# Performance work log

Measured on AMD Instinct MI355X. Metric: run time of the kernel, lower is better.

The kernel has to match this reference:

```python
import jax, jax.numpy as jnp
import numpy as np

H = W = 56; WS = 7; SHIFT = 3; HEADS = 4; DIM = 128
HD = DIM // HEADS; SCALE = HD ** -0.5
NW = (H // WS) * (W // WS)  # 64 windows per image
N = WS * WS                 # 49 tokens per window
HID = int(DIM * 4.0)


def _rel_index():
    coords = np.stack(np.meshgrid(np.arange(WS), np.arange(WS), indexing='ij'))  # (2,WS,WS)
    cf = coords.reshape(2, -1)
    rel = (cf[:, :, None] - cf[:, None, :]).transpose(1, 2, 0)  # (N,N,2)
    rel[:, :, 0] += WS - 1
    rel[:, :, 1] += WS - 1
    rel[:, :, 0] *= 2 * WS - 1
    return jnp.asarray(rel.sum(-1))  # (N,N) int indices into bias table


def _attn_mask():
    img = np.zeros((H, W))
    cnt = 0
    for hs in (slice(0, -WS), slice(-WS, -SHIFT), slice(-SHIFT, None)):
        for ws in (slice(0, -WS), slice(-WS, -SHIFT), slice(-SHIFT, None)):
            img[hs, ws] = cnt
            cnt += 1
    mw = img.reshape(H // WS, WS, W // WS, WS).transpose(0, 2, 1, 3).reshape(-1, N)
    diff = mw[:, None, :] - mw[:, :, None]
    return jnp.asarray(np.where(diff != 0, -100.0, 0.0).astype(np.float32))  # (NW,N,N)

REL_IDX = _rel_index()
ATTN_MASK = _attn_mask()


def _ln(x, g, b):
    m = jnp.mean(x, -1, keepdims=True)
    v = jnp.var(x, -1, keepdims=True)
    return (x - m) * jax.lax.rsqrt(v + 1e-5) * g + b


def _win_part(x):  # (B,H,W,C) -> (B*NW, N, C)
    B = x.shape[0]
    x = x.reshape(B, H // WS, WS, W // WS, WS, DIM)
    return x.transpose(0, 1, 3, 2, 4, 5).reshape(-1, N, DIM)


def _win_rev(x, B):  # (B*NW, N, C) -> (B,H,W,C)
    x = x.reshape(B, H // WS, W // WS, WS, WS, DIM)
    return x.transpose(0, 1, 3, 2, 4, 5).reshape(B, H, W, DIM)


def setup_inputs() -> dict:
    key = jax.random.key(0)
    ks = jax.random.split(key, 8)
    s = 0.02
    return {
        'x': jax.random.normal(ks[0], (64, H * W, DIM), jnp.float32),
        'g1': jnp.ones((DIM,), jnp.float32),
        'b1': jnp.zeros((DIM,), jnp.float32),
        'qkv_w': jax.random.normal(ks[1], (3 * DIM, DIM), jnp.float32) * s,
        'qkv_b': jnp.zeros((3 * DIM,), jnp.float32),
        'rpb_table': jax.random.normal(ks[2], ((2 * WS - 1) ** 2, HEADS), jnp.float32) * s,
        'proj_w': jax.random.normal(ks[3], (DIM, DIM), jnp.float32) * s,
        'proj_b': jnp.zeros((DIM,), jnp.float32),
        'g2': jnp.ones((DIM,), jnp.float32),
        'b2': jnp.zeros((DIM,), jnp.float32),
        'fc1_w': jax.random.normal(ks[4], (HID, DIM), jnp.float32) * s,
        'fc1_b': jnp.zeros((HID,), jnp.float32),
        'fc2_w': jax.random.normal(ks[5], (DIM, HID), jnp.float32) * s,
        'fc2_b': jnp.zeros((DIM,), jnp.float32),
    }


def reference(x, g1, b1, qkv_w, qkv_b, rpb_table, proj_w, proj_b, g2, b2, fc1_w, fc1_b, fc2_w, fc2_b):
    B = x.shape[0]
    shortcut = x
    h = _ln(x, g1, b1).reshape(B, H, W, DIM)
    # cyclic shift + window partition
    h = jnp.roll(h, shift=(-SHIFT, -SHIFT), axis=(1, 2))
    xw = _win_part(h)  # (B*NW, N, C)
    B_ = xw.shape[0]
    # window attention
    qkv = (xw @ qkv_w.T + qkv_b).reshape(B_, N, 3, HEADS, HD).transpose(2, 0, 3, 1, 4)
    q, k, v = qkv[0] * SCALE, qkv[1], qkv[2]  # (B_, heads, N, hd)
    attn = jnp.einsum('bhnd,bhmd->bhnm', q, k)
    bias = rpb_table[REL_IDX.reshape(-1)].reshape(N, N, HEADS).transpose(2, 0, 1)  # (heads,N,N)
    attn = attn + bias[None]
    attn = attn.reshape(B, NW, HEADS, N, N) + ATTN_MASK[None, :, None]
    attn = jax.nn.softmax(attn.reshape(B_, HEADS, N, N), axis=-1)
    out = jnp.einsum('bhnm,bhmd->bhnd', attn, v).transpose(0, 2, 1, 3).reshape(B_, N, DIM)
    out = out @ proj_w.T + proj_b
    # reverse windows + reverse shift
    h = _win_rev(out, B)
    h = jnp.roll(h, shift=(SHIFT, SHIFT), axis=(1, 2)).reshape(B, H * W, DIM)
    x = shortcut + h
    # MLP
    y = _ln(x, g2, b2)
    y = jax.nn.gelu(y @ fc1_w.T + fc1_b, approximate=False)
    y = y @ fc2_w.T + fc2_b
    return x + y
```

## Files before the change

### kernel.cpp

```cpp
#include <hip/hip_runtime.h>

typedef unsigned int uint;
typedef unsigned short ushort;
using short8 = __attribute__((ext_vector_type(8))) short;
using f32x4  = __attribute__((ext_vector_type(4))) float;
using uint4v = __attribute__((ext_vector_type(4))) uint;

#define SCALE_ 0.17677669529663687f
#define MFMA(a,b,c) __builtin_amdgcn_mfma_f32_16x16x32_bf16(a,b,c,0,0,0)

__device__ inline ushort f2bf(float f){
  uint u = __float_as_uint(f);
  return (ushort)((u + 0x7fffu + ((u >> 16) & 1u)) >> 16);
}
__device__ inline uint pk2(float a, float b){
  return (uint)f2bf(a) | ((uint)f2bf(b) << 16);
}
__device__ inline float gelu(float v){
  return 0.5f * v * (1.f + erff(v * 0.70710678f));
}

__global__ __launch_bounds__(256) void prep_kernel(
    const float* __restrict__ qkv_w, const float* __restrict__ qkv_b,
    const float* __restrict__ rpb, const float* __restrict__ proj_w,
    const float* __restrict__ fc1_w, const float* __restrict__ fc2_w,
    ushort* __restrict__ qkv_wb, float* __restrict__ qkv_bs,
    ushort* __restrict__ proj_wb, ushort* __restrict__ fc1_wb,
    ushort* __restrict__ fc2_wb, ushort* __restrict__ T2b)
{
  int i = blockIdx.x * 256 + threadIdx.x;
  if (i < 49152) qkv_wb[i] = f2bf(qkv_w[i] * (i < 16384 ? SCALE_ : 1.f));
  if (i < 16384) proj_wb[i] = f2bf(proj_w[i]);
  if (i < 65536) { fc1_wb[i] = f2bf(fc1_w[i]); fc2_wb[i] = f2bf(fc2_w[i]); }
  if (i < 384)   qkv_bs[i] = qkv_b[i] * (i < 128 ? SCALE_ : 1.f);
  if (i < 65536) {
    int cls = i >> 14, h = (i >> 12) & 3, tok = (i >> 6) & 63, key = i & 63;
    float val = -30000.f;
    if (tok < 49 && key < 49) {
      int ri = tok / 7, ci = tok - ri * 7, rj = key / 7, cj = key - rj * 7;
      val = rpb[((ri - rj + 6) * 13 + (ci - cj + 6)) * 4 + h];
      int er = cls >> 1, ec = cls & 1;
      int regi = (er ? (ri < 4 ? 1 : 2) : 0) * 3 + (ec ? (ci < 4 ? 1 : 2) : 0);
      int regj = (er ? (rj < 4 ? 1 : 2) : 0) * 3 + (ec ? (cj < 4 ? 1 : 2) : 0);
      if (regi != regj) val -= 100.f;
    }
    T2b[i] = f2bf(val);
  }
}

__global__ __launch_bounds__(256, 2) void attn_kernel(
    const float* __restrict__ x, const float* __restrict__ g1, const float* __restrict__ b1,
    const ushort* __restrict__ qkv_wb, const float* __restrict__ qkv_bs,
    const ushort* __restrict__ T2b, const ushort* __restrict__ proj_wb,
    const float* __restrict__ proj_b, float* __restrict__ x_new)
{
  __shared__ __align__(16) char smem[25088];
  char*   xls = smem;
  ushort* oa  = (ushort*)smem;
  float*  Rp  = (float*)smem;
  const int tid = threadIdx.x;
  const int w = tid >> 6, lane = tid & 63;
  const int g = lane >> 4, li = lane & 15;
  const int blk = blockIdx.x;
  const int b = blk >> 6, wi = blk & 63;
  const int wr = wi >> 3, wc = wi & 7;
  const float* xb = x + (size_t)b * (3136 * 128);
  const f32x4 zf = {0.f, 0.f, 0.f, 0.f};
  const int srcA = ((g & 1) << 5) + li;
  const int srcB = srcA + 16;
  const int hi = g >> 1;

#pragma unroll
  for (int it = 0; it < 7; ++it) {
    int gi = it * 256 + tid;
    bool ok = gi < 1568;
    int t = ok ? (gi >> 5) : 48;
    int ch4 = (gi & 31) << 2;
    int tr = t / 7, tc = t - tr * 7;
    int rr = wr * 7 + tr + 3; rr -= (rr >= 56) ? 56 : 0;
    int cc = wc * 7 + tc + 3; cc -= (cc >= 56) ? 56 : 0;
    float4 v = *(const float4*)(xb + (size_t)(rr * 56 + cc) * 128 + ch4);
    float s = v.x + v.y + v.z + v.w;
    float s2 = v.x*v.x + v.y*v.y + v.z*v.z + v.w*v.w;
#pragma unroll
    for (int off = 16; off; off >>= 1) { s += __shfl_xor(s, off); s2 += __shfl_xor(s2, off); }
    float mn = s * 0.0078125f;
    float rs = rsqrtf(s2 * 0.0078125f - mn * mn + 1e-5f);
    if (ok) {
      float4 gg = *(const float4*)(g1 + ch4);
      float4 bb = *(const float4*)(b1 + ch4);
      uint2 u;
      u.x = pk2((v.x - mn) * rs * gg.x + bb.x, (v.y - mn) * rs * gg.y + bb.y);
      u.y = pk2((v.z - mn) * rs * gg.z + bb.z, (v.w - mn) * rs * gg.w + bb.w);
      int slot = ch4 >> 3;
      int tokx = t ^ ((slot & 7) << 1);
      *(uint2*)(xls + (slot * 64 + tokx) * 16 + ((ch4 & 4) << 1)) = u;
    }
  }
  if (tid < 240) {
    int slot = tid & 15, t = 49 + (tid >> 4);
    int tokx = t ^ ((slot & 7) << 1);
    uint4 z = make_uint4(0u, 0u, 0u, 0u);
    *(uint4*)(xls + (slot * 64 + tokx) * 16) = z;
  }
  __syncthreads();

  short8 kf[4];
  {
    f32x4 kacc[2][4];
#pragma unroll
    for (int cf = 0; cf < 2; ++cf)
#pragma unroll
      for (int m = 0; m < 4; ++m) kacc[cf][m] = zf;
#pragma unroll
    for (int kt = 0; kt < 4; ++kt) {
      const int slot = kt * 4 + g;
      short8 xf[4];
#pragma unroll
      for (int m = 0; m < 4; ++m)
        xf[m] = *(const short8*)(xls + (slot * 64 + ((m * 16 + li) ^ ((slot & 7) << 1))) * 16);
      const int wofs = kt * 32 + g * 8;
#pragma unroll
      for (int cf = 0; cf < 2; ++cf) {
        short8 wk = *(const short8*)(qkv_wb + (size_t)(128 + w * 32 + cf * 16 + li) * 128 + wofs);
#pragma unroll
        for (int m = 0; m < 4; ++m) kacc[cf][m] = MFMA(wk, xf[m], kacc[cf][m]);
      }
    }
    uint2 kp[2][4];
#pragma unroll
    for (int cf = 0; cf < 2; ++cf) {
      f32x4 kb4 = *(const f32x4*)(qkv_bs + 128 + w * 32 + cf * 16 + g * 4);
#pragma unroll
      for (int m = 0; m < 4; ++m) {
        f32x4 kv = kacc[cf][m] + kb4;
        kp[cf][m].x = pk2(kv[0], kv[1]); kp[cf][m].y = pk2(kv[2], kv[3]);
      }
    }
#pragma unroll
    for (int n = 0; n < 4; ++n) {
      uint a0 = __shfl(kp[0][n].x, srcA), a1 = __shfl(kp[0][n].y, srcA);
      uint a2 = __shfl(kp[0][n].x, srcB), a3 = __shfl(kp[0][n].y, srcB);
      uint b0 = __shfl(kp[1][n].x, srcA), b1 = __shfl(kp[1][n].y, srcA);
      uint b2 = __shfl(kp[1][n].x, srcB), b3 = __shfl(kp[1][n].y, srcB);
      uint4v u = { hi ? b0 : a0, hi ? b1 : a1, hi ? b2 : a2, hi ? b3 : a3 };
      kf[n] = __builtin_bit_cast(short8, u);
    }
  }

  short8 vt[2][2];
  {
    f32x4 vacc[4][2];
#pragma unroll
    for (int m = 0; m < 4; ++m) { vacc[m][0] = zf; vacc[m][1] = zf; }
#pragma unroll
    for (int kt = 0; kt < 4; ++kt) {
      const int slot = kt * 4 + g;
      short8 xf[4];
#pragma unroll
      for (int m = 0; m < 4; ++m)
        xf[m] = *(const short8*)(xls + (slot * 64 + ((m * 16 + li) ^ ((slot & 7) << 1))) * 16);
      const int wofs = kt * 32 + g * 8;
#pragma unroll
      for (int cf = 0; cf < 2; ++cf) {
        short8 wv = *(const short8*)(qkv_wb + (size_t)(256 + w * 32 + cf * 16 + li) * 128 + wofs);
#pragma unroll
        for (int m = 0; m < 4; ++m) vacc[m][cf] = MFMA(xf[m], wv, vacc[m][cf]);
      }
    }
    uint2 vp[4][2];
#pragma unroll
    for (int cf = 0; cf < 2; ++cf) {
      float vb = qkv_bs[256 + w * 32 + cf * 16 + li];
#pragma unroll
      for (int m = 0; m < 4; ++m) {
        f32x4 vv = vacc[m][cf];
        vp[m][cf].x = pk2(vv[0] + vb, vv[1] + vb);
        vp[m][cf].y = pk2(vv[2] + vb, vv[3] + vb);
      }
    }
#pragma unroll
    for (int kt = 0; kt < 2; ++kt)
#pragma unroll
      for (int half = 0; half < 2; ++half) {
        uint a0 = __shfl(vp[kt * 2][half].x, srcA), a1 = __shfl(vp[kt * 2][half].y, srcA);
        uint a2 = __shfl(vp[kt * 2][half].x, srcB), a3 = __shfl(vp[kt * 2][half].y, srcB);
        uint b0 = __shfl(vp[kt * 2 + 1][half].x, srcA), b1 = __shfl(vp[kt * 2 + 1][half].y, srcA);
        uint b2 = __shfl(vp[kt * 2 + 1][half].x, srcB), b3 = __shfl(vp[kt * 2 + 1][half].y, srcB);
        uint4v uv = { hi ? b0 : a0, hi ? b1 : a1, hi ? b2 : a2, hi ? b3 : a3 };
        vt[kt][half] = __builtin_bit_cast(short8, uv);
      }
  }

  f32x4 oacc[2][4];
#pragma unroll
  for (int cf = 0; cf < 2; ++cf)
#pragma unroll
    for (int m = 0; m < 4; ++m) oacc[cf][m] = zf;
  {
    const int cls = ((wr == 7) ? 2 : 0) | ((wc == 7) ? 1 : 0);
    const ushort* Tb = T2b + ((cls * 4 + w) << 12);
    const f32x4 qb40 = *(const f32x4*)(qkv_bs + w * 32 + g * 4);
    const f32x4 qb41 = *(const f32x4*)(qkv_bs + w * 32 + 16 + g * 4);
#pragma unroll
    for (int m = 0; m < 4; ++m) {
      f32x4 qacc[2] = {zf, zf};
#pragma unroll
      for (int kt = 0; kt < 4; ++kt) {
        const int slot = kt * 4 + g;
        short8 xfm = *(const short8*)(xls + (slot * 64 + ((m * 16 + li) ^ ((slot & 7) << 1))) * 16);
        const int wofs = kt * 32 + g * 8;
        short8 wq0 = *(const short8*)(qkv_wb + (size_t)(w * 32 + li) * 128 + wofs);
        short8 wq1 = *(const short8*)(qkv_wb + (size_t)(w * 32 + 16 + li) * 128 + wofs);
        qacc[0] = MFMA(wq0, xfm, qacc[0]);
        qacc[1] = MFMA(wq1, xfm, qacc[1]);
      }
      uint2 qpm[2];
      {
        f32x4 q0 = qacc[0] + qb40;
        f32x4 q1 = qacc[1] + qb41;
        qpm[0].x = pk2(q0[0], q0[1]); qpm[0].y = pk2(q0[2], q0[3]);
        qpm[1].x = pk2(q1[0], q1[1]); qpm[1].y = pk2(q1[2], q1[3]);
      }
      uint a0 = __shfl(qpm[0].x, srcA), a1 = __shfl(qpm[0].y, srcA);
      uint a2 = __shfl(qpm[0].x, srcB), a3 = __shfl(qpm[0].y, srcB);
      uint b0 = __shfl(qpm[1].x, srcA), b1 = __shfl(qpm[1].y, srcA);
      uint b2 = __shfl(qpm[1].x, srcB), b3 = __shfl(qpm[1].y, srcB);
      uint4v uq = { hi ? b0 : a0, hi ? b1 : a1, hi ? b2 : a2, hi ? b3 : a3 };
      short8 qf = __builtin_bit_cast(short8, uq);
      f32x4 s[4];
#pragma unroll
      for (int n = 0; n < 4; ++n) {
        s[n] = MFMA(kf[n], qf, zf);
        uint2 tv = *(const uint2*)(Tb + (m * 16 + li) * 64 + n * 16 + g * 4);
        s[n][0] += __uint_as_float(tv.x << 16);
        s[n][1] += __uint_as_float(tv.x & 0xffff0000u);
        s[n][2] += __uint_as_float(tv.y << 16);
        s[n][3] += __uint_as_float(tv.y & 0xffff0000u);
      }
      float mx = -3.4e38f;
#pragma unroll
      for (int n = 0; n < 4; ++n)
        mx = fmaxf(mx, fmaxf(fmaxf(s[n][0], s[n][1]), fmaxf(s[n][2], s[n][3])));
      mx = fmaxf(mx, __shfl_xor(mx, 16));
      mx = fmaxf(mx, __shfl_xor(mx, 32));
      float sum = 0.f;
#pragma unroll
      for (int n = 0; n < 4; ++n)
#pragma unroll
        for (int r = 0; r < 4; ++r) { float e = __expf(s[n][r] - mx); s[n][r] = e; sum += e; }
      sum += __shfl_xor(sum, 16); sum += __shfl_xor(sum, 32);
      float rsm = 1.f / sum;
      uint um[4][2];
#pragma unroll
      for (int n = 0; n < 4; ++n) {
        um[n][0] = pk2(s[n][0] * rsm, s[n][1] * rsm);
        um[n][1] = pk2(s[n][2] * rsm, s[n][3] * rsm);
      }
#pragma unroll
      for (int kt = 0; kt < 2; ++kt) {
        uint t00 = __shfl(um[kt * 2][0], srcA),  t10 = __shfl(um[kt * 2 + 1][0], srcA);
        uint t01 = __shfl(um[kt * 2][1], srcA),  t11 = __shfl(um[kt * 2 + 1][1], srcA);
        uint t02 = __shfl(um[kt * 2][0], srcB),  t12 = __shfl(um[kt * 2 + 1][0], srcB);
        uint t03 = __shfl(um[kt * 2][1], srcB),  t13 = __shfl(um[kt * 2 + 1][1], srcB);
        uint4v pu = { hi ? t10 : t00, hi ? t11 : t01, hi ? t12 : t02, hi ? t13 : t03 };
        short8 pf = __builtin_bit_cast(short8, pu);
        oacc[0][m] = MFMA(vt[kt][0], pf, oacc[0][m]);
        oacc[1][m] = MFMA(vt[kt][1], pf, oacc[1][m]);
      }
    }
  }
  __syncthreads();
#pragma unroll
  for (int cf = 0; cf < 2; ++cf)
#pragma unroll
    for (int m = 0; m < 4; ++m) {
      uint2 ou; ou.x = pk2(oacc[cf][m][0], oacc[cf][m][1]);
      ou.y = pk2(oacc[cf][m][2], oacc[cf][m][3]);
      *(uint2*)((char*)oa + ((m * 16 + li) * 136 + w * 32 + cf * 16 + g * 4) * 2) = ou;
    }
  __syncthreads();

  f32x4 pacc[2][4];
#pragma unroll
  for (int cf = 0; cf < 2; ++cf)
#pragma unroll
    for (int m = 0; m < 4; ++m) pacc[cf][m] = zf;
#pragma unroll
  for (int kt = 0; kt < 4; ++kt) {
    short8 af[4];
#pragma unroll
    for (int m = 0; m < 4; ++m)
      af[m] = *(const short8*)((char*)oa + (m * 16 + li) * 272 + kt * 64 + g * 16);
#pragma unroll
    for (int cf = 0; cf < 2; ++cf) {
      short8 wp = *(const short8*)(proj_wb + (size_t)(w * 32 + cf * 16 + li) * 128 + kt * 32 + g * 8);
#pragma unroll
      for (int m = 0; m < 4; ++m) pacc[cf][m] = MFMA(af[m], wp, pacc[cf][m]);
    }
  }
  __syncthreads();
#pragma unroll
  for (int cf = 0; cf < 2; ++cf) {
    int col = w * 32 + cf * 16 + li;
    float pb = proj_b[col];
#pragma unroll
    for (int m = 0; m < 4; ++m)
#pragma unroll
      for (int r = 0; r < 4; ++r) {
        int t2 = m * 16 + g * 4 + r;
        if (t2 < 49)
          Rp[t2 * 128 + (col ^ ((t2 & 7) << 2))] = pacc[cf][m][r] + pb;
      }
  }
  __syncthreads();

#pragma unroll
  for (int it = 0; it < 7; ++it) {
    int gi = it * 256 + tid;
    if (gi < 1568) {
      int t = gi >> 5, ch4 = (gi & 31) << 2;
      int tr = t / 7, tc = t - tr * 7;
      int rr = wr * 7 + tr + 3; rr -= (rr >= 56) ? 56 : 0;
      int cc = wc * 7 + tc + 3; cc -= (cc >= 56) ? 56 : 0;
      size_t off = ((size_t)b * 3136 + rr * 56 + cc) * 128 + ch4;
      f32x4 d = *(const f32x4*)&Rp[t * 128 + (ch4 ^ ((t & 7) << 2))];
      float4 xr = *(const float4*)(x + off);
      float4 ov;
      ov.x = xr.x + d[0]; ov.y = xr.y + d[1];
      ov.z = xr.z + d[2]; ov.w = xr.w + d[3];
      *(float4*)(x_new + off) = ov;
    }
  }
}

__global__ __launch_bounds__(256, 2) void mlp_kernel(
    float* __restrict__ xio,
    const float* __restrict__ g2, const float* __restrict__ b2,
    const ushort* __restrict__ w1, const float* __restrict__ fb1,
    const ushort* __restrict__ w2, const float* __restrict__ fb2)
{
  __shared__ __align__(16) char smem[32768];
  char* Axs = smem;
  char* hls = smem + 16384;
  float* Rp = (float*)smem;
  const int tid = threadIdx.x, lane = tid & 63, w = tid >> 6;
  const int g = lane >> 4, li = lane & 15;
  float* xw = xio + (size_t)blockIdx.x * 64 * 128;
  const f32x4 zf = {0.f, 0.f, 0.f, 0.f};

#pragma unroll
  for (int it = 0; it < 8; ++it) {
    int gi = it * 256 + tid;
    int row = gi >> 5, ch4 = (gi & 31) << 2;
    float4 v = *(const float4*)(xw + row * 128 + ch4);
    float s = v.x + v.y + v.z + v.w;
    float s2 = v.x*v.x + v.y*v.y + v.z*v.z + v.w*v.w;
#pragma unroll
    for (int off = 16; off; off >>= 1) { s += __shfl_xor(s, off); s2 += __shfl_xor(s2, off); }
    float mn = s * 0.0078125f;
    float rs = rsqrtf(s2 * 0.0078125f - mn * mn + 1e-5f);
    float4 gg = *(const float4*)(g2 + ch4);
    float4 bb = *(const float4*)(b2 + ch4);
    uint2 u;
    u.x = pk2((v.x - mn) * rs * gg.x + bb.x, (v.y - mn) * rs * gg.y + bb.y);
    u.y = pk2((v.z - mn) * rs * gg.z + bb.z, (v.w - mn) * rs * gg.w + bb.w);
    int slot = ch4 >> 3;
    int tokx = row ^ ((slot & 7) << 1);
    *(uint2*)(Axs + (slot * 64 + tokx) * 16 + ((ch4 & 4) << 1)) = u;
  }
  __syncthreads();

  f32x4 acc2[4][2];
#pragma unroll
  for (int mi = 0; mi < 4; ++mi) { acc2[mi][0] = zf; acc2[mi][1] = zf; }

  for (int ck = 0; ck < 4; ++ck) {
    f32x4 acc1[2][4];
#pragma unroll
    for (int oi = 0; oi < 2; ++oi)
#pragma unroll
      for (int mi = 0; mi < 4; ++mi) acc1[oi][mi] = zf;
#pragma unroll
    for (int kt = 0; kt < 4; ++kt) {
      const int slot = kt * 4 + g;
      short8 xf[4];
#pragma unroll
      for (int mi = 0; mi < 4; ++mi)
        xf[mi] = *(const short8*)(Axs + (slot * 64 + ((mi * 16 + li) ^ ((slot & 7) << 1))) * 16);
#pragma unroll
      for (int oi = 0; oi < 2; ++oi) {
        short8 wf = *(const short8*)(w1 + (size_t)(ck * 128 + w * 32 + oi * 16 + li) * 128 + kt * 32 + g * 8);
#pragma unroll
        for (int mi = 0; mi < 4; ++mi) acc1[oi][mi] = MFMA(wf, xf[mi], acc1[oi][mi]);
      }
    }
#pragma unroll
    for (int oi = 0; oi < 2; ++oi) {
      f32x4 b4 = *(const f32x4*)(fb1 + ck * 128 + w * 32 + oi * 16 + g * 4);
#pragma unroll
      for (int mi = 0; mi < 4; ++mi) {
        f32x4 h = acc1[oi][mi] + b4;
        uint2 u; u.x = pk2(gelu(h[0]), gelu(h[1])); u.y = pk2(gelu(h[2]), gelu(h[3]));
        *(uint2*)(hls + ((w * 4 + oi * 2 + (g >> 1)) * 64 + mi * 16 + li) * 16 + ((g & 1) << 3)) = u;
      }
    }
    __syncthreads();
#pragma unroll
    for (int kt = 0; kt < 4; ++kt) {
      short8 hf[4];
#pragma unroll
      for (int mi = 0; mi < 4; ++mi)
        hf[mi] = *(const short8*)(hls + ((kt * 4 + g) * 64 + mi * 16 + li) * 16);
#pragma unroll
      for (int bo = 0; bo < 2; ++bo) {
        short8 wf = *(const short8*)(w2 + (size_t)(w * 32 + bo * 16 + li) * 512 + ck * 128 + kt * 32 + g * 8);
#pragma unroll
        for (int mi = 0; mi < 4; ++mi) acc2[mi][bo] = MFMA(hf[mi], wf, acc2[mi][bo]);
      }
    }
    __syncthreads();
  }

#pragma unroll
  for (int mi = 0; mi < 4; ++mi)
#pragma unroll
    for (int bo = 0; bo < 2; ++bo) {
      int out = w * 32 + bo * 16 + li;
#pragma unroll
      for (int r = 0; r < 4; ++r) {
        int tok = mi * 16 + g * 4 + r;
        Rp[tok * 128 + (out ^ ((tok & 7) << 2))] = acc2[mi][bo][r];
      }
    }
  __syncthreads();
#pragma unroll
  for (int it = 0; it < 8; ++it) {
    int gi = it * 256 + tid;
    int row = gi >> 5, ch4 = (gi & 31) << 2;
    f32x4 d = *(const f32x4*)&Rp[row * 128 + (ch4 ^ ((row & 7) << 2))];
    float4 xr = *(const float4*)(xw + row * 128 + ch4);
    float4 bb = *(const float4*)(fb2 + ch4);
    float4 ov;
    ov.x = xr.x + d[0] + bb.x; ov.y = xr.y + d[1] + bb.y;
    ov.z = xr.z + d[2] + bb.z; ov.w = xr.w + d[3] + bb.w;
    *(float4*)(xw + row * 128 + ch4) = ov;
  }
}

extern "C" void kernel_launch(void* const* d_in, const int* in_sizes, int n_in,
                              void* d_out, int out_size, void* d_ws, size_t ws_size,
                              hipStream_t stream)
{
  const float* x      = (const float*)d_in[0];
  const float* g1     = (const float*)d_in[1];
  const float* b1     = (const float*)d_in[2];
  const float* qkv_w  = (const float*)d_in[3];
  const float* qkv_b  = (const float*)d_in[4];
  const float* rpb    = (const float*)d_in[5];
  const float* proj_w = (const float*)d_in[6];
  const float* proj_b = (const float*)d_in[7];
  const float* g2     = (const float*)d_in[8];
  const float* b2     = (const float*)d_in[9];
  const float* fc1_w  = (const float*)d_in[10];
  const float* fc1_b  = (const float*)d_in[11];
  const float* fc2_w  = (const float*)d_in[12];
  const float* fc2_b  = (const float*)d_in[13];

  char* ws = (char*)d_ws;
  ushort* T2b     = (ushort*)ws;
  ushort* qkv_wb  = (ushort*)(ws + 262144);
  ushort* proj_wb = (ushort*)(ws + 360448);
  ushort* fc1_wb  = (ushort*)(ws + 393216);
  ushort* fc2_wb  = (ushort*)(ws + 524288);
  float*  qkv_bs  = (float*)(ws + 655360);
  float* out = (float*)d_out;

  prep_kernel<<<256, 256, 0, stream>>>(qkv_w, qkv_b, rpb, proj_w, fc1_w, fc2_w,
                                       qkv_wb, qkv_bs, proj_wb, fc1_wb, fc2_wb, T2b);
  attn_kernel<<<4096, 256, 0, stream>>>(x, g1, b1, qkv_wb, qkv_bs, T2b,
                                        proj_wb, proj_b, out);
  mlp_kernel<<<3136, 256, 0, stream>>>(out, g2, b2, fc1_wb, fc1_b, fc2_wb, fc2_b);
}
```

Before: 317.1 us.

## Run window attention with one wavefront per window, looping over heads

The attention kernel now launches 64 threads per block, and one wavefront processes all four heads of a window in sequence. Block-wide barriers go away, and the head outputs are regrouped with cross-lane shuffles for the projection instead of being staged through shared memory. The projection result is now kept in shared memory as bf16 rather than fp32, which shrinks shared memory use but adds rounding before the residual add. The cost is more serial work per wave, higher register pressure from holding all heads' outputs, and possibly lower occupancy or latency hiding.

```diff
diff --git a/kernel.cpp b/kernel.cpp
--- a/kernel.cpp
+++ b/kernel.cpp
@@ -16,6 +16,8 @@
 __device__ inline uint pk2(float a, float b){
   return (uint)f2bf(a) | ((uint)f2bf(b) << 16);
 }
+__device__ inline float bf2f_lo(uint u){ return __uint_as_float(u << 16); }
+__device__ inline float bf2f_hi(uint u){ return __uint_as_float(u & 0xffff0000u); }
 __device__ inline float gelu(float v){
   return 0.5f * v * (1.f + erff(v * 0.70710678f));
 }
@@ -48,18 +50,16 @@
   }
 }
 
-__global__ __launch_bounds__(256, 2) void attn_kernel(
+__global__ __launch_bounds__(64, 2) void attn_kernel(
     const float* __restrict__ x, const float* __restrict__ g1, const float* __restrict__ b1,
     const ushort* __restrict__ qkv_wb, const float* __restrict__ qkv_bs,
     const ushort* __restrict__ T2b, const ushort* __restrict__ proj_wb,
     const float* __restrict__ proj_b, float* __restrict__ x_new)
 {
-  __shared__ __align__(16) char smem[25088];
+  __shared__ __align__(16) char smem[16384];
   char*   xls = smem;
-  ushort* oa  = (ushort*)smem;
-  float*  Rp  = (float*)smem;
-  const int tid = threadIdx.x;
-  const int w = tid >> 6, lane = tid & 63;
+  ushort* Rpb = (ushort*)smem;
+  const int lane = threadIdx.x;
   const int g = lane >> 4, li = lane & 15;
   const int blk = blockIdx.x;
   const int b = blk >> 6, wi = blk & 63;
@@ -69,10 +69,11 @@
   const int srcA = ((g & 1) << 5) + li;
   const int srcB = srcA + 16;
   const int hi = g >> 1;
-
-#pragma unroll
-  for (int it = 0; it < 7; ++it) {
-    int gi = it * 256 + tid;
+  const int cls = ((wr == 7) ? 2 : 0) | ((wc == 7) ? 1 : 0);
+
+#pragma unroll
+  for (int it = 0; it < 25; ++it) {
+    int gi = it * 64 + lane;
     bool ok = gi < 1568;
     int t = ok ? (gi >> 5) : 48;
     int ch4 = (gi & 31) << 2;
@@ -97,238 +98,251 @@
       *(uint2*)(xls + (slot * 64 + tokx) * 16 + ((ch4 & 4) << 1)) = u;
     }
   }
-  if (tid < 240) {
-    int slot = tid & 15, t = 49 + (tid >> 4);
-    int tokx = t ^ ((slot & 7) << 1);
-    uint4 z = make_uint4(0u, 0u, 0u, 0u);
-    *(uint4*)(xls + (slot * 64 + tokx) * 16) = z;
-  }
-  __syncthreads();
-
-  short8 kf[4];
-  {
-    f32x4 kacc[2][4];
-#pragma unroll
-    for (int cf = 0; cf < 2; ++cf)
-#pragma unroll
-      for (int m = 0; m < 4; ++m) kacc[cf][m] = zf;
-#pragma unroll
-    for (int kt = 0; kt < 4; ++kt) {
-      const int slot = kt * 4 + g;
-      short8 xf[4];
-#pragma unroll
-      for (int m = 0; m < 4; ++m)
-        xf[m] = *(const short8*)(xls + (slot * 64 + ((m * 16 + li) ^ ((slot & 7) << 1))) * 16);
-      const int wofs = kt * 32 + g * 8;
-#pragma unroll
-      for (int cf = 0; cf < 2; ++cf) {
-        short8 wk = *(const short8*)(qkv_wb + (size_t)(128 + w * 32 + cf * 16 + li) * 128 + wofs);
-#pragma unroll
-        for (int m = 0; m < 4; ++m) kacc[cf][m] = MFMA(wk, xf[m], kacc[cf][m]);
-      }
-    }
-    uint2 kp[2][4];
-#pragma unroll
-    for (int cf = 0; cf < 2; ++cf) {
-      f32x4 kb4 = *(const f32x4*)(qkv_bs + 128 + w * 32 + cf * 16 + g * 4);
-#pragma unroll
-      for (int m = 0; m < 4; ++m) {
-        f32x4 kv = kacc[cf][m] + kb4;
-        kp[cf][m].x = pk2(kv[0], kv[1]); kp[cf][m].y = pk2(kv[2], kv[3]);
-      }
-    }
-#pragma unroll
-    for (int n = 0; n < 4; ++n) {
-      uint a0 = __shfl(kp[0][n].x, srcA), a1 = __shfl(kp[0][n].y, srcA);
-      uint a2 = __shfl(kp[0][n].x, srcB), a3 = __shfl(kp[0][n].y, srcB);
-      uint b0 = __shfl(kp[1][n].x, srcA), b1 = __shfl(kp[1][n].y, srcA);
-      uint b2 = __shfl(kp[1][n].x, srcB), b3 = __shfl(kp[1][n].y, srcB);
-      uint4v u = { hi ? b0 : a0, hi ? b1 : a1, hi ? b2 : a2, hi ? b3 : a3 };
-      kf[n] = __builtin_bit_cast(short8, u);
-    }
-  }
-
-  short8 vt[2][2];
-  {
-    f32x4 vacc[4][2];
-#pragma unroll
-    for (int m = 0; m < 4; ++m) { vacc[m][0] = zf; vacc[m][1] = zf; }
-#pragma unroll
-    for (int kt = 0; kt < 4; ++kt) {
-      const int slot = kt * 4 + g;
-      short8 xf[4];
-#pragma unroll
-      for (int m = 0; m < 4; ++m)
-        xf[m] = *(const short8*)(xls + (slot * 64 + ((m * 16 + li) ^ ((slot & 7) << 1))) * 16);
-      const int wofs = kt * 32 + g * 8;
-#pragma unroll
-      for (int cf = 0; cf < 2; ++cf) {
-        short8 wv = *(const short8*)(qkv_wb + (size_t)(256 + w * 32 + cf * 16 + li) * 128 + wofs);
-#pragma unroll
-        for (int m = 0; m < 4; ++m) vacc[m][cf] = MFMA(xf[m], wv, vacc[m][cf]);
-      }
-    }
-    uint2 vp[4][2];
-#pragma unroll
-    for (int cf = 0; cf < 2; ++cf) {
-      float vb = qkv_bs[256 + w * 32 + cf * 16 + li];
-#pragma unroll
-      for (int m = 0; m < 4; ++m) {
-        f32x4 vv = vacc[m][cf];
-        vp[m][cf].x = pk2(vv[0] + vb, vv[1] + vb);
-        vp[m][cf].y = pk2(vv[2] + vb, vv[3] + vb);
-      }
-    }
-#pragma unroll
-    for (int kt = 0; kt < 2; ++kt)
-#pragma unroll
-      for (int half = 0; half < 2; ++half) {
-        uint a0 = __shfl(vp[kt * 2][half].x, srcA), a1 = __shfl(vp[kt * 2][half].y, srcA);
-        uint a2 = __shfl(vp[kt * 2][half].x, srcB), a3 = __shfl(vp[kt * 2][half].y, srcB);
-        uint b0 = __shfl(vp[kt * 2 + 1][half].x, srcA), b1 = __shfl(vp[kt * 2 + 1][half].y, srcA);
-        uint b2 = __shfl(vp[kt * 2 + 1][half].x, srcB), b3 = __shfl(vp[kt * 2 + 1][half].y, srcB);
-        uint4v uv = { hi ? b0 : a0, hi ? b1 : a1, hi ? b2 : a2, hi ? b3 : a3 };
-        vt[kt][half] = __builtin_bit_cast(short8, uv);
-      }
-  }
-
-  f32x4 oacc[2][4];
-#pragma unroll
-  for (int cf = 0; cf < 2; ++cf)
-#pragma unroll
-    for (int m = 0; m < 4; ++m) oacc[cf][m] = zf;
-  {
-    const int cls = ((wr == 7) ? 2 : 0) | ((wc == 7) ? 1 : 0);
-    const ushort* Tb = T2b + ((cls * 4 + w) << 12);
-    const f32x4 qb40 = *(const f32x4*)(qkv_bs + w * 32 + g * 4);
-    const f32x4 qb41 = *(const f32x4*)(qkv_bs + w * 32 + 16 + g * 4);
-#pragma unroll
-    for (int m = 0; m < 4; ++m) {
-      f32x4 qacc[2] = {zf, zf};
+#pragma unroll
+  for (int i0 = 0; i0 < 4; ++i0) {
+    int i = i0 * 64 + lane;
+    if (i < 240) {
+      int slot = i & 15, t = 49 + (i >> 4);
+      int tokx = t ^ ((slot & 7) << 1);
+      uint4 z = make_uint4(0u, 0u, 0u, 0u);
+      *(uint4*)(xls + (slot * 64 + tokx) * 16) = z;
+    }
+  }
+
+  uint2 opk[4][4][2];
+#pragma unroll
+  for (int h = 0; h < 4; ++h) {
+    short8 kf[4];
+    {
+      f32x4 kacc[2][4];
+#pragma unroll
+      for (int cf = 0; cf < 2; ++cf)
+#pragma unroll
+        for (int m = 0; m < 4; ++m) kacc[cf][m] = zf;
 #pragma unroll
       for (int kt = 0; kt < 4; ++kt) {
         const int slot = kt * 4 + g;
-        short8 xfm = *(const short8*)(xls + (slot * 64 + ((m * 16 + li) ^ ((slot & 7) << 1))) * 16);
+        short8 xf[4];
+#pragma unroll
+        for (int m = 0; m < 4; ++m)
+          xf[m] = *(const short8*)(xls + (slot * 64 + ((m * 16 + li) ^ ((slot & 7) << 1))) * 16);
         const int wofs = kt * 32 + g * 8;
-        short8 wq0 = *(const short8*)(qkv_wb + (size_t)(w * 32 + li) * 128 + wofs);
-        short8 wq1 = *(const short8*)(qkv_wb + (size_t)(w * 32 + 16 + li) * 128 + wofs);
-        qacc[0] = MFMA(wq0, xfm, qacc[0]);
-        qacc[1] = MFMA(wq1, xfm, qacc[1]);
-      }
-      uint2 qpm[2];
-      {
-        f32x4 q0 = qacc[0] + qb40;
-        f32x4 q1 = qacc[1] + qb41;
-        qpm[0].x = pk2(q0[0], q0[1]); qpm[0].y = pk2(q0[2], q0[3]);
-        qpm[1].x = pk2(q1[0], q1[1]); qpm[1].y = pk2(q1[2], q1[3]);
-      }
-      uint a0 = __shfl(qpm[0].x, srcA), a1 = __shfl(qpm[0].y, srcA);
-      uint a2 = __shfl(qpm[0].x, srcB), a3 = __shfl(qpm[0].y, srcB);
-      uint b0 = __shfl(qpm[1].x, srcA), b1 = __shfl(qpm[1].y, srcA);
-      uint b2 = __shfl(qpm[1].x, srcB), b3 = __shfl(qpm[1].y, srcB);
-      uint4v uq = { hi ? b0 : a0, hi ? b1 : a1, hi ? b2 : a2, hi ? b3 : a3 };
-      short8 qf = __builtin_bit_cast(short8, uq);
-      f32x4 s[4];
+#pragma unroll
+        for (int cf = 0; cf < 2; ++cf) {
+          short8 wk = *(const short8*)(qkv_wb + (size_t)(128 + h * 32 + cf * 16 + li) * 128 + wofs);
+#pragma unroll
+          for (int m = 0; m < 4; ++m) kacc[cf][m] = MFMA(wk, xf[m], kacc[cf][m]);
+        }
+      }
+      uint2 kp[2][4];
+#pragma unroll
+      for (int cf = 0; cf < 2; ++cf) {
+        f32x4 kb4 = *(const f32x4*)(qkv_bs + 128 + h * 32 + cf * 16 + g * 4);
+#pragma unroll
+        for (int m = 0; m < 4; ++m) {
+          f32x4 kv = kacc[cf][m] + kb4;
+          kp[cf][m].x = pk2(kv[0], kv[1]); kp[cf][m].y = pk2(kv[2], kv[3]);
+        }
+      }
 #pragma unroll
       for (int n = 0; n < 4; ++n) {
-        s[n] = MFMA(kf[n], qf, zf);
-        uint2 tv = *(const uint2*)(Tb + (m * 16 + li) * 64 + n * 16 + g * 4);
-        s[n][0] += __uint_as_float(tv.x << 16);
-        s[n][1] += __uint_as_float(tv.x & 0xffff0000u);
-        s[n][2] += __uint_as_float(tv.y << 16);
-        s[n][3] += __uint_as_float(tv.y & 0xffff0000u);
-      }
-      float mx = -3.4e38f;
-#pragma unroll
-      for (int n = 0; n < 4; ++n)
-        mx = fmaxf(mx, fmaxf(fmaxf(s[n][0], s[n][1]), fmaxf(s[n][2], s[n][3])));
-      mx = fmaxf(mx, __shfl_xor(mx, 16));
-      mx = fmaxf(mx, __shfl_xor(mx, 32));
-      float sum = 0.f;
-#pragma unroll
-      for (int n = 0; n < 4; ++n)
-#pragma unroll
-        for (int r = 0; r < 4; ++r) { float e = __expf(s[n][r] - mx); s[n][r] = e; sum += e; }
-      sum += __shfl_xor(sum, 16); sum += __shfl_xor(sum, 32);
-      float rsm = 1.f / sum;
-      uint um[4][2];
-#pragma unroll
-      for (int n = 0; n < 4; ++n) {
-        um[n][0] = pk2(s[n][0] * rsm, s[n][1] * rsm);
-        um[n][1] = pk2(s[n][2] * rsm, s[n][3] * rsm);
-      }
-#pragma unroll
-      for (int kt = 0; kt < 2; ++kt) {
-        uint t00 = __shfl(um[kt * 2][0], srcA),  t10 = __shfl(um[kt * 2 + 1][0], srcA);
-        uint t01 = __shfl(um[kt * 2][1], srcA),  t11 = __shfl(um[kt * 2 + 1][1], srcA);
-        uint t02 = __shfl(um[kt * 2][0], srcB),  t12 = __shfl(um[kt * 2 + 1][0], srcB);
-        uint t03 = __shfl(um[kt * 2][1], srcB),  t13 = __shfl(um[kt * 2 + 1][1], srcB);
-        uint4v pu = { hi ? t10 : t00, hi ? t11 : t01, hi ? t12 : t02, hi ? t13 : t03 };
-        short8 pf = __builtin_bit_cast(short8, pu);
-        oacc[0][m] = MFMA(vt[kt][0], pf, oacc[0][m]);
-        oacc[1][m] = MFMA(vt[kt][1], pf, oacc[1][m]);
-      }
-    }
-  }
-  __syncthreads();
-#pragma unroll
-  for (int cf = 0; cf < 2; ++cf)
-#pragma unroll
-    for (int m = 0; m < 4; ++m) {
-      uint2 ou; ou.x = pk2(oacc[cf][m][0], oacc[cf][m][1]);
-      ou.y = pk2(oacc[cf][m][2], oacc[cf][m][3]);
-      *(uint2*)((char*)oa + ((m * 16 + li) * 136 + w * 32 + cf * 16 + g * 4) * 2) = ou;
-    }
-  __syncthreads();
-
-  f32x4 pacc[2][4];
-#pragma unroll
-  for (int cf = 0; cf < 2; ++cf)
-#pragma unroll
-    for (int m = 0; m < 4; ++m) pacc[cf][m] = zf;
-#pragma unroll
-  for (int kt = 0; kt < 4; ++kt) {
-    short8 af[4];
+        uint a0 = __shfl(kp[0][n].x, srcA), a1 = __shfl(kp[0][n].y, srcA);
+        uint a2 = __shfl(kp[0][n].x, srcB), a3 = __shfl(kp[0][n].y, srcB);
+        uint b0 = __shfl(kp[1][n].x, srcA), b1 = __shfl(kp[1][n].y, srcA);
+        uint b2 = __shfl(kp[1][n].x, srcB), b3 = __shfl(kp[1][n].y, srcB);
+        uint4v u = { hi ? b0 : a0, hi ? b1 : a1, hi ? b2 : a2, hi ? b3 : a3 };
+        kf[n] = __builtin_bit_cast(short8, u);
+      }
+    }
+    short8 vt[2][2];
+    {
+      f32x4 vacc[4][2];
+#pragma unroll
+      for (int m = 0; m < 4; ++m) { vacc[m][0] = zf; vacc[m][1] = zf; }
+#pragma unroll
+      for (int kt = 0; kt < 4; ++kt) {
+        const int slot = kt * 4 + g;
+        short8 xf[4];
+#pragma unroll
+        for (int m = 0; m < 4; ++m)
+          xf[m] = *(const short8*)(xls + (slot * 64 + ((m * 16 + li) ^ ((slot & 7) << 1))) * 16);
+        const int wofs = kt * 32 + g * 8;
+#pragma unroll
+        for (int cf = 0; cf < 2; ++cf) {
+          short8 wv = *(const short8*)(qkv_wb + (size_t)(256 + h * 32 + cf * 16 + li) * 128 + wofs);
+#pragma unroll
+          for (int m = 0; m < 4; ++m) vacc[m][cf] = MFMA(xf[m], wv, vacc[m][cf]);
+        }
+      }
+      uint2 vp[4][2];
+#pragma unroll
+      for (int cf = 0; cf < 2; ++cf) {
+        float vb = qkv_bs[256 + h * 32 + cf * 16 + li];
+#pragma unroll
+        for (int m = 0; m < 4; ++m) {
+          f32x4 vv = vacc[m][cf];
+          vp[m][cf].x = pk2(vv[0] + vb, vv[1] + vb);
+          vp[m][cf].y = pk2(vv[2] + vb, vv[3] + vb);
+        }
+      }
+#pragma unroll
+      for (int kt = 0; kt < 2; ++kt)
+#pragma unroll
+        for (int half = 0; half < 2; ++half) {
+          uint a0 = __shfl(vp[kt * 2][half].x, srcA), a1 = __shfl(vp[kt * 2][half].y, srcA);
+          uint a2 = __shfl(vp[kt * 2][half].x, srcB), a3 = __shfl(vp[kt * 2][half].y, srcB);
+          uint b0 = __shfl(vp[kt * 2 + 1][half].x, srcA), b1 = __shfl(vp[kt * 2 + 1][half].y, srcA);
+          uint b2 = __shfl(vp[kt * 2 + 1][half].x, srcB), b3 = __shfl(vp[kt * 2 + 1][half].y, srcB);
+          uint4v uv = { hi ? b0 : a0, hi ? b1 : a1, hi ? b2 : a2, hi ? b3 : a3 };
+          vt[kt][half] = __builtin_bit_cast(short8, uv);
+        }
+    }
+    f32x4 oacc[2][4];
+#pragma unroll
+    for (int cf = 0; cf < 2; ++cf)
+#pragma unroll
+      for (int m = 0; m < 4; ++m) oacc[cf][m] = zf;
+    {
+      const ushort* Tb = T2b + ((cls * 4 + h) << 12);
+      const f32x4 qb40 = *(const f32x4*)(qkv_bs + h * 32 + g * 4);
+      const f32x4 qb41 = *(const f32x4*)(qkv_bs + h * 32 + 16 + g * 4);
+#pragma unroll
+      for (int m = 0; m < 4; ++m) {
+        f32x4 qacc[2] = {zf, zf};
+#pragma unroll
+        for (int kt = 0; kt < 4; ++kt) {
+          const int slot = kt * 4 + g;
+          short8 xfm = *(const short8*)(xls + (slot * 64 + ((m * 16 + li) ^ ((slot & 7) << 1))) * 16);
+          const int wofs = kt * 32 + g * 8;
+          short8 wq0 = *(const short8*)(qkv_wb + (size_t)(h * 32 + li) * 128 + wofs);
+          short8 wq1 = *(const short8*)(qkv_wb + (size_t)(h * 32 + 16 + li) * 128 + wofs);
+          qacc[0] = MFMA(wq0, xfm, qacc[0]);
+          qacc[1] = MFMA(wq1, xfm, qacc[1]);
+        }
+        uint2 qpm[2];
+        {
+          f32x4 q0 = qacc[0] + qb40;
+          f32x4 q1 = qacc[1] + qb41;
+          qpm[0].x = pk2(q0[0], q0[1]); qpm[0].y = pk2(q0[2], q0[3]);
+          qpm[1].x = pk2(q1[0], q1[1]); qpm[1].y = pk2(q1[2], q1[3]);
+        }
+        uint a0 = __shfl(qpm[0].x, srcA), a1 = __shfl(qpm[0].y, srcA);
+        uint a2 = __shfl(qpm[0].x, srcB), a3 = __shfl(qpm[0].y, srcB);
+        uint b0 = __shfl(qpm[1].x, srcA), b1 = __shfl(qpm[1].y, srcA);
+        uint b2 = __shfl(qpm[1].x, srcB), b3 = __shfl(qpm[1].y, srcB);
+        uint4v uq = { hi ? b0 : a0, hi ? b1 : a1, hi ? b2 : a2, hi ? b3 : a3 };
+        short8 qf = __builtin_bit_cast(short8, uq);
+        f32x4 s[4];
+#pragma unroll
+        for (int n = 0; n < 4; ++n) {
+          s[n] = MFMA(kf[n], qf, zf);
+          uint2 tv = *(const uint2*)(Tb + (m * 16 + li) * 64 + n * 16 + g * 4);
+          s[n][0] += bf2f_lo(tv.x);
+          s[n][1] += bf2f_hi(tv.x);
+          s[n][2] += bf2f_lo(tv.y);
+          s[n][3] += bf2f_hi(tv.y);
+        }
+        float mx = -3.4e38f;
+#pragma unroll
+        for (int n = 0; n < 4; ++n)
+          mx = fmaxf(mx, fmaxf(fmaxf(s[n][0], s[n][1]), fmaxf(s[n][2], s[n][3])));
+        mx = fmaxf(mx, __shfl_xor(mx, 16));
+        mx = fmaxf(mx, __shfl_xor(mx, 32));
+        float sum = 0.f;
+#pragma unroll
+        for (int n = 0; n < 4; ++n)
+#pragma unroll
+          for (int r = 0; r < 4; ++r) { float e = __expf(s[n][r] - mx); s[n][r] = e; sum += e; }
+        sum += __shfl_xor(sum, 16); sum += __shfl_xor(sum, 32);
+        float rsm = 1.f / sum;
+        uint um[4][2];
+#pragma unroll
+        for (int n = 0; n < 4; ++n) {
+          um[n][0] = pk2(s[n][0] * rsm, s[n][1] * rsm);
+          um[n][1] = pk2(s[n][2] * rsm, s[n][3] * rsm);
+        }
+#pragma unroll
+        for (int kt = 0; kt < 2; ++kt) {
+          uint t00 = __shfl(um[kt * 2][0], srcA),  t10 = __shfl(um[kt * 2 + 1][0], srcA);
+          uint t01 = __shfl(um[kt * 2][1], srcA),  t11 = __shfl(um[kt * 2 + 1][1], srcA);
+          uint t02 = __shfl(um[kt * 2][0], srcB),  t12 = __shfl(um[kt * 2 + 1][0], srcB);
+          uint t03 = __shfl(um[kt * 2][1], srcB),  t13 = __shfl(um[kt * 2 + 1][1], srcB);
+          uint4v pu = { hi ? t10 : t00, hi ? t11 : t01, hi ? t12 : t02, hi ? t13 : t03 };
+          short8 pf = __builtin_bit_cast(short8, pu);
+          oacc[0][m] = MFMA(vt[kt][0], pf, oacc[0][m]);
+          oacc[1][m] = MFMA(vt[kt][1], pf, oacc[1][m]);
+        }
+      }
+    }
 #pragma unroll
     for (int m = 0; m < 4; ++m)
-      af[m] = *(const short8*)((char*)oa + (m * 16 + li) * 272 + kt * 64 + g * 16);
+#pragma unroll
+      for (int cf = 0; cf < 2; ++cf) {
+        opk[h][m][cf].x = pk2(oacc[cf][m][0], oacc[cf][m][1]);
+        opk[h][m][cf].y = pk2(oacc[cf][m][2], oacc[cf][m][3]);
+      }
+  }
+
+  short8 bf_[4][4];
+#pragma unroll
+  for (int m = 0; m < 4; ++m)
+#pragma unroll
+    for (int kt = 0; kt < 4; ++kt) {
+      uint a0 = __shfl(opk[kt][m][0].x, srcA), a1 = __shfl(opk[kt][m][0].y, srcA);
+      uint a2 = __shfl(opk[kt][m][0].x, srcB), a3 = __shfl(opk[kt][m][0].y, srcB);
+      uint b0 = __shfl(opk[kt][m][1].x, srcA), b1 = __shfl(opk[kt][m][1].y, srcA);
+      uint b2 = __shfl(opk[kt][m][1].x, srcB), b3 = __shfl(opk[kt][m][1].y, srcB);
+      uint4v u = { hi ? b0 : a0, hi ? b1 : a1, hi ? b2 : a2, hi ? b3 : a3 };
+      bf_[m][kt] = __builtin_bit_cast(short8, u);
+    }
+
+#pragma unroll
+  for (int cfp = 0; cfp < 4; ++cfp) {
+    f32x4 pacc[2][4];
+#pragma unroll
+    for (int cf = 0; cf < 2; ++cf)
+#pragma unroll
+      for (int m = 0; m < 4; ++m) pacc[cf][m] = zf;
+#pragma unroll
+    for (int kt = 0; kt < 4; ++kt) {
+#pragma unroll
+      for (int cf = 0; cf < 2; ++cf) {
+        short8 wp = *(const short8*)(proj_wb + (size_t)(cfp * 32 + cf * 16 + li) * 128 + kt * 32 + g * 8);
+#pragma unroll
+        for (int m = 0; m < 4; ++m) pacc[cf][m] = MFMA(wp, bf_[m][kt], pacc[cf][m]);
+      }
+    }
 #pragma unroll
     for (int cf = 0; cf < 2; ++cf) {
-      short8 wp = *(const short8*)(proj_wb + (size_t)(w * 32 + cf * 16 + li) * 128 + kt * 32 + g * 8);
-#pragma unroll
-      for (int m = 0; m < 4; ++m) pacc[cf][m] = MFMA(af[m], wp, pacc[cf][m]);
-    }
-  }
-  __syncthreads();
-#pragma unroll
-  for (int cf = 0; cf < 2; ++cf) {
-    int col = w * 32 + cf * 16 + li;
-    float pb = proj_b[col];
-#pragma unroll
-    for (int m = 0; m < 4; ++m)
-#pragma unroll
-      for (int r = 0; r < 4; ++r) {
-        int t2 = m * 16 + g * 4 + r;
-        if (t2 < 49)
-          Rp[t2 * 128 + (col ^ ((t2 & 7) << 2))] = pacc[cf][m][r] + pb;
-      }
-  }
-  __syncthreads();
-
-#pragma unroll
-  for (int it = 0; it < 7; ++it) {
-    int gi = it * 256 + tid;
+      int och0 = cfp * 32 + cf * 16 + g * 4;
+      f32x4 pb4 = *(const f32x4*)(proj_b + och0);
+#pragma unroll
+      for (int m = 0; m < 4; ++m) {
+        int t = m * 16 + li;
+        if (t < 49) {
+          uint2 ou;
+          ou.x = pk2(pacc[cf][m][0] + pb4[0], pacc[cf][m][1] + pb4[1]);
+          ou.y = pk2(pacc[cf][m][2] + pb4[2], pacc[cf][m][3] + pb4[3]);
+          *(uint2*)((char*)Rpb + (t * 136 + och0) * 2) = ou;
+        }
+      }
+    }
+  }
+
+#pragma unroll
+  for (int it = 0; it < 25; ++it) {
+    int gi = it * 64 + lane;
     if (gi < 1568) {
       int t = gi >> 5, ch4 = (gi & 31) << 2;
       int tr = t / 7, tc = t - tr * 7;
       int rr = wr * 7 + tr + 3; rr -= (rr >= 56) ? 56 : 0;
       int cc = wc * 7 + tc + 3; cc -= (cc >= 56) ? 56 : 0;
       size_t off = ((size_t)b * 3136 + rr * 56 + cc) * 128 + ch4;
-      f32x4 d = *(const f32x4*)&Rp[t * 128 + (ch4 ^ ((t & 7) << 2))];
+      uint2 du = *(const uint2*)((char*)Rpb + (t * 136 + ch4) * 2);
       float4 xr = *(const float4*)(x + off);
       float4 ov;
-      ov.x = xr.x + d[0]; ov.y = xr.y + d[1];
-      ov.z = xr.z + d[2]; ov.w = xr.w + d[3];
+      ov.x = xr.x + bf2f_lo(du.x); ov.y = xr.y + bf2f_hi(du.x);
+      ov.z = xr.z + bf2f_lo(du.y); ov.w = xr.w + bf2f_hi(du.y);
       *(float4*)(x_new + off) = ov;
     }
   }
@@ -478,7 +492,7 @@
 
   prep_kernel<<<256, 256, 0, stream>>>(qkv_w, qkv_b, rpb, proj_w, fc1_w, fc2_w,
                                        qkv_wb, qkv_bs, proj_wb, fc1_wb, fc2_wb, T2b);
-  attn_kernel<<<4096, 256, 0, stream>>>(x, g1, b1, qkv_wb, qkv_bs, T2b,
-                                        proj_wb, proj_b, out);
+  attn_kernel<<<4096, 64, 0, stream>>>(x, g1, b1, qkv_wb, qkv_bs, T2b,
+                                       proj_wb, proj_b, out);
   mlp_kernel<<<3136, 256, 0, stream>>>(out, g2, b2, fc1_wb, fc1_b, fc2_wb, fc2_b);
 }
```

Result: slower. 350.7 us (+10.6%).
